# Kernel tuning notes

Hardware: AMD Instinct MI355X
Metric: run time of the kernel (lower is better)

## Reference

```python
import jax, jax.numpy as jnp
import numpy as np

NUM_GRAPHS = 5 * 0 + 64  # number of graphs in the batch
NUM_CLASSES = 5


def gcn_conv(x, src, dst, W, b, n_nodes):
    """PyG GCNConv: x' = D^{-1/2} (A+I) D^{-1/2} x W + b (self-loops already in src/dst)."""
    h = x @ W  # [N, out]
    deg = jax.ops.segment_sum(jnp.ones(dst.shape, h.dtype), dst, num_segments=n_nodes)
    dinv = deg ** -0.5  # deg >= 1 thanks to self-loops
    norm = dinv[src] * dinv[dst]  # [E+N]
    msg = h[src] * norm[:, None]  # gather + normalize
    out = jax.ops.segment_sum(msg, dst, num_segments=n_nodes)  # scatter-add
    return out + b


def setup_inputs() -> dict:
    key = jax.random.key(0)
    ks = jax.random.split(key, 12)
    N, E, D_IN, D_H, D_F = 50000, 500000, 128, 256, 256
    x = jax.random.normal(ks[0], (N, D_IN), dtype=jnp.float32)
    edge_index = jax.random.randint(ks[1], (2, E), 0, N, dtype=jnp.int64)
    batch = jnp.sort(jax.random.randint(ks[2], (N,), 0, NUM_GRAPHS, dtype=jnp.int64))
    def lin(k, fi, fo):
        s = 1.0 / np.sqrt(fi)
        return jax.random.uniform(k, (fi, fo), jnp.float32, -s, s)
    return {
        "x": x, "edge_index": edge_index, "batch": batch,
        "W0": lin(ks[3], D_IN, D_H), "b0": jnp.zeros((D_H,), jnp.float32),
        "W1": lin(ks[4], D_H, D_H),  "b1": jnp.zeros((D_H,), jnp.float32),
        "W2": lin(ks[5], D_H, D_H),  "b2": jnp.zeros((D_H,), jnp.float32),
        "Wc1": lin(ks[6], D_H, D_F), "bc1": jnp.zeros((D_F,), jnp.float32),
        "Wc2": lin(ks[7], D_F, NUM_CLASSES), "bc2": jnp.zeros((NUM_CLASSES,), jnp.float32),
    }


def reference(x, edge_index, batch, W0, b0, W1, b1, W2, b2, Wc1, bc1, Wc2, bc2):
    n_nodes = x.shape[0]
    loops = jnp.arange(n_nodes, dtype=edge_index.dtype)
    src = jnp.concatenate([edge_index[0], loops])
    dst = jnp.concatenate([edge_index[1], loops])

    h = jax.nn.relu(gcn_conv(x, src, dst, W0, b0, n_nodes))
    h = jax.nn.relu(gcn_conv(h, src, dst, W1, b1, n_nodes))
    h = jax.nn.relu(gcn_conv(h, src, dst, W2, b2, n_nodes))

    # global_mean_pool over batch ids
    sums = jax.ops.segment_sum(h, batch, num_segments=NUM_GRAPHS)
    cnts = jax.ops.segment_sum(jnp.ones((n_nodes,), h.dtype), batch, num_segments=NUM_GRAPHS)
    g = sums / jnp.maximum(cnts, 1.0)[:, None]  # [NUM_GRAPHS, D_H]

    # classifier MLP (dropout inactive at eval)
    out = jax.nn.relu(g @ Wc1 + bc1) @ Wc2 + bc2
    return out
```

## Files before the change

### kernel.cpp

```cpp
#include <hip/hip_runtime.h>
#include <hip/hip_fp16.h>

typedef _Float16 f16x8 __attribute__((ext_vector_type(8)));
typedef float fx4 __attribute__((ext_vector_type(4)));

#define AS_G(p) ((const __attribute__((address_space(1))) void*)(p))
#define AS_L(p) ((__attribute__((address_space(3))) void*)(p))

struct __align__(8) half4 { __half2 lo, hi; };
struct __align__(8) edge_t { int u; float w; };

__device__ inline void split2h(float a, __half& hi, __half& lo) {
    hi = __float2half(a);
    lo = __float2half(a - __half2float(hi));
}


__global__ void k_degx(const int* __restrict__ dst, int E, int* __restrict__ deg, int degB,
                       const float* __restrict__ x, __half* __restrict__ xh, int nx) {
    if (blockIdx.x < (unsigned)degB) {
        int i = (blockIdx.x * 256 + threadIdx.x) * 4;
        if (i + 4 <= E) {
            int4 d4 = *(const int4*)&dst[i];
            atomicAdd(&deg[d4.x], 1);
            atomicAdd(&deg[d4.y], 1);
            atomicAdd(&deg[d4.z], 1);
            atomicAdd(&deg[d4.w], 1);
        } else {
            for (int j = i; j < E; ++j) atomicAdd(&deg[dst[j]], 1);
        }
    } else {
        int i = (blockIdx.x - degB) * 1024 + threadIdx.x * 4;
        if (i < nx) {
            float4 v = *(const float4*)&x[i];
            __half2 h0(__float2half(v.x), __float2half(v.y));
            __half2 h1(__float2half(v.z), __float2half(v.w));
            *(__half2*)&xh[i] = h0;
            *(__half2*)&xh[i + 2] = h1;
        }
    }
}

__global__ void k_scan1w(const int* __restrict__ deg, int N, int nb,
                         int* __restrict__ part, int* __restrict__ bsum, float* __restrict__ dinv,
                         const float* __restrict__ W0, __half* __restrict__ h0, __half* __restrict__ l0,
                         const float* __restrict__ W1, __half* __restrict__ h1, __half* __restrict__ l1,
                         const float* __restrict__ W2, __half* __restrict__ h2, __half* __restrict__ l2,
                         int DIN, int DH) {
    __shared__ int s[256];
    if (blockIdx.x < (unsigned)nb) {
        int i = blockIdx.x * 256 + threadIdx.x;
        int v = (i < N) ? deg[i] : 0;
        if (i < N) dinv[i] = 1.0f / sqrtf((float)(v + 1));
        s[threadIdx.x] = v;
        __syncthreads();
        for (int off = 1; off < 256; off <<= 1) {
            int t = (threadIdx.x >= off) ? s[threadIdx.x - off] : 0;
            __syncthreads();
            s[threadIdx.x] += t;
            __syncthreads();
        }
        if (i < N) part[i] = s[threadIdx.x] - v;
        if (threadIdx.x == 255) bsum[blockIdx.x] = s[255];
    } else {
        int i = (blockIdx.x - nb) * 256 + threadIdx.x;
        const int n0 = DIN * DH, n1 = DH * DH;
        const float* W; __half *hT, *lT; int K, li;
        if (i < n0) { W = W0; hT = h0; lT = l0; K = DIN; li = i; }
        else if (i < n0 + n1) { W = W1; hT = h1; lT = l1; K = DH; li = i - n0; }
        else if (i < n0 + 2 * n1) { W = W2; hT = h2; lT = l2; K = DH; li = i - n0 - n1; }
        else return;
        int k = li / DH, n = li - k * DH;
        __half h, l;
        split2h(W[li], h, l);
        hT[(size_t)n * K + k] = h;
        lT[(size_t)n * K + k] = l;
    }
}

__global__ void k_scan3(const int* __restrict__ part, const int* __restrict__ bsum, int nb,
                        int N, int E, int* __restrict__ rowptr, int* __restrict__ cursor) {
    __shared__ int s[256];
    const int t = threadIdx.x;
    s[t] = (t < nb && t < (int)blockIdx.x) ? bsum[t] : 0;
    __syncthreads();
    for (int off = 128; off > 0; off >>= 1) {
        if (t < off) s[t] += s[t + off];
        __syncthreads();
    }
    const int base = s[0];
    int i = blockIdx.x * 256 + t;
    if (i < N) {
        int v = part[i] + base;
        rowptr[i] = v;
        cursor[i] = v;
    }
    if (i == 0) rowptr[N] = E;
}

__global__ void k_fill(const int* __restrict__ src, const int* __restrict__ dst, int E,
                       const float* __restrict__ dinv, int* __restrict__ cursor,
                       edge_t* __restrict__ edg) {
    int e = blockIdx.x * blockDim.x + threadIdx.x;
    if (e < E) {
        int s = src[e], d = dst[e];
        int p = atomicAdd(&cursor[d], 1);
        edge_t ed;
        ed.u = s;
        ed.w = dinv[s] * dinv[d];
        edg[p] = ed;
    }
}


__device__ __forceinline__ void gemm_core(
    const __half* __restrict__ Aop, const __half* __restrict__ BhiT, const __half* __restrict__ BloT,
    __half* smem, int Nrows, int K, int row0,
    int wid, int lane, int wrow, int wcol, int quad, int l16, fx4 (&acc)[4][4]) {
    const __half* gp[5];
    int ldsoff[5];
#pragma unroll
    for (int j = 0; j < 5; ++j) {
        int L = wid * 5 + j;
        int arr, slot;
        if (L < 8) { arr = 0; slot = L; }
        else if (L < 24) { arr = 1; slot = L - 8; }
        else { arr = 2; slot = L - 24; }
        int r = 16 * slot + (lane >> 2);
        int s = lane & 3;
        int q = (s - (r >> 1)) & 3;
        const __half* garr = (arr == 0) ? Aop : (arr == 1) ? BhiT : BloT;
        int grow = (arr == 0) ? min(row0 + r, Nrows - 1) : r;
        gp[j] = garr + (size_t)grow * K + q * 8;
        ldsoff[j] = ((arr == 0) ? 0 : (arr == 1) ? 8192 : 24576) + slot * 1024;
    }

    const __half* sA   = smem;
    const __half* sBhi = smem + 4096;
    const __half* sBlo = smem + 12288;

    int aidx[4], bidx[4];
#pragma unroll
    for (int t = 0; t < 4; ++t) {
        int ra = wrow * 64 + t * 16 + l16;
        aidx[t] = ra * 32 + ((quad + (ra >> 1)) & 3) * 8;
        int rb = wcol * 64 + t * 16 + l16;
        bidx[t] = rb * 32 + ((quad + (rb >> 1)) & 3) * 8;
    }

    for (int k0 = 0; k0 < K; k0 += 32) {
#pragma unroll
        for (int j = 0; j < 5; ++j)
            __builtin_amdgcn_global_load_lds(AS_G(gp[j] + k0), AS_L((char*)smem + ldsoff[j]), 16, 0, 0);
        __syncthreads();

        f16x8 a[4];
#pragma unroll
        for (int mi = 0; mi < 4; ++mi) a[mi] = *(const f16x8*)&sA[aidx[mi]];
#pragma unroll
        for (int nj = 0; nj < 4; ++nj) {
            f16x8 bh = *(const f16x8*)&sBhi[bidx[nj]];
            f16x8 bl = *(const f16x8*)&sBlo[bidx[nj]];
#pragma unroll
            for (int mi = 0; mi < 4; ++mi) {
                acc[mi][nj] = __builtin_amdgcn_mfma_f32_16x16x32_f16(a[mi], bh, acc[mi][nj], 0, 0, 0);
                acc[mi][nj] = __builtin_amdgcn_mfma_f32_16x16x32_f16(a[mi], bl, acc[mi][nj], 0, 0, 0);
            }
        }
        __syncthreads();
    }
}

__global__ __launch_bounds__(512) void k_gemm_mfma(
    const __half* __restrict__ Aop, const __half* __restrict__ BhiT, const __half* __restrict__ BloT,
    const float* __restrict__ bias, __half* __restrict__ C, int Nrows, int K) {
    __shared__ __align__(16) __half smem[20480];
    const int tid = threadIdx.x;
    const int wid = tid >> 6, lane = tid & 63;
    const int row0 = blockIdx.x * 128;
    const int wrow = wid & 1, wcol = wid >> 1;
    const int quad = lane >> 4, l16 = lane & 15;

    fx4 acc[4][4] = {};
    gemm_core(Aop, BhiT, BloT, smem, Nrows, K, row0, wid, lane, wrow, wcol, quad, l16, acc);

#pragma unroll
    for (int mi = 0; mi < 4; ++mi) {
        const int rbase = row0 + wrow * 64 + mi * 16 + quad * 4;
#pragma unroll
        for (int nj = 0; nj < 4; ++nj) {
            const int c = wcol * 64 + nj * 16 + l16;
            const float bc = bias[c];
#pragma unroll
            for (int reg = 0; reg < 4; ++reg) {
                int r = rbase + reg;
                if (r < Nrows) C[(size_t)r * 256 + c] = __float2half(fmaxf(acc[mi][nj][reg] + bc, 0.f));
            }
        }
    }
}

__global__ __launch_bounds__(512) void k_gemm_pool(
    const __half* __restrict__ Aop, const __half* __restrict__ BhiT, const __half* __restrict__ BloT,
    const float* __restrict__ bias, const int* __restrict__ batch,
    float* __restrict__ gsum, int Nrows, int K) {
    __shared__ __align__(16) __half smem[20480];
    const int tid = threadIdx.x;
    const int wid = tid >> 6, lane = tid & 63;
    const int row0 = blockIdx.x * 128;
    const int wrow = wid & 1, wcol = wid >> 1;
    const int quad = lane >> 4, l16 = lane & 15;

    fx4 acc[4][4] = {};
    gemm_core(Aop, BhiT, BloT, smem, Nrows, K, row0, wid, lane, wrow, wcol, quad, l16, acc);

    int bg[4][4];
#pragma unroll
    for (int mi = 0; mi < 4; ++mi)
#pragma unroll
        for (int reg = 0; reg < 4; ++reg) {
            int r = row0 + wrow * 64 + mi * 16 + quad * 4 + reg;
            bg[mi][reg] = (r < Nrows) ? batch[r] : -1;
        }
    const int gfirst = batch[row0 < Nrows ? row0 : (Nrows - 1)];
    const int glast  = batch[min(row0 + 127, Nrows - 1)];

#pragma unroll
    for (int nj = 0; nj < 4; ++nj) {
        const int c = wcol * 64 + nj * 16 + l16;
        const float bc = bias[c];
        for (int g = gfirst; g <= glast; ++g) {
            float s = 0.f;
#pragma unroll
            for (int mi = 0; mi < 4; ++mi)
#pragma unroll
                for (int reg = 0; reg < 4; ++reg)
                    if (bg[mi][reg] == g) s += fmaxf(acc[mi][nj][reg] + bc, 0.f);
            s += __shfl_xor(s, 16);
            s += __shfl_xor(s, 32);
            if (quad == 0) atomicAdd(&gsum[g * 256 + c], s);
        }
    }
}


__global__ __launch_bounds__(256) void k_agg256(const __half* __restrict__ H, const int* __restrict__ rowptr,
                                                const edge_t* __restrict__ edg,
                                                const float* __restrict__ dinv,
                                                __half* __restrict__ outA, int N) {
    const int wave = threadIdx.x >> 6, lane = threadIdx.x & 63;
    const int v = blockIdx.x * 4 + wave;
    if (v >= N) return;

    const float di = dinv[v];
    const float selfn = di * di;
    half4 hv = ((const half4*)&H[(size_t)v * 256])[lane];
    float2 s0 = __half22float2(hv.lo), s1 = __half22float2(hv.hi);
    float ax = selfn * s0.x, ay = selfn * s0.y, az = selfn * s1.x, aw = selfn * s1.y;

    int e = rowptr[v];
    const int end = rowptr[v + 1];
    for (; e + 8 <= end; e += 8) {
        edge_t ed[8]; half4 g[8];
#pragma unroll
        for (int j = 0; j < 8; ++j) ed[j] = edg[e + j];
#pragma unroll
        for (int j = 0; j < 8; ++j) g[j] = ((const half4*)&H[(size_t)ed[j].u * 256])[lane];
#pragma unroll
        for (int j = 0; j < 8; ++j) {
            float2 f0 = __half22float2(g[j].lo), f1 = __half22float2(g[j].hi);
            ax += ed[j].w * f0.x; ay += ed[j].w * f0.y; az += ed[j].w * f1.x; aw += ed[j].w * f1.y;
        }
    }
    for (; e < end; ++e) {
        edge_t ed = edg[e];
        half4 g = ((const half4*)&H[(size_t)ed.u * 256])[lane];
        float2 f0 = __half22float2(g.lo), f1 = __half22float2(g.hi);
        ax += ed.w * f0.x; ay += ed.w * f0.y; az += ed.w * f1.x; aw += ed.w * f1.y;
    }

    half4 o;
    o.lo = __floats2half2_rn(ax, ay);
    o.hi = __floats2half2_rn(az, aw);
    ((half4*)outA)[(size_t)v * 64 + lane] = o;
}

__global__ __launch_bounds__(256) void k_agg128(const __half* __restrict__ X, const int* __restrict__ rowptr,
                                                const edge_t* __restrict__ edg,
                                                const float* __restrict__ dinv,
                                                __half* __restrict__ outA, int N) {
    const int half = threadIdx.x >> 5, sub = threadIdx.x & 31;
    const int v = blockIdx.x * 8 + half;
    if (v >= N) return;

    const float di = dinv[v];
    const float selfn = di * di;
    half4 hv = ((const half4*)&X[(size_t)v * 128])[sub];
    float2 s0 = __half22float2(hv.lo), s1 = __half22float2(hv.hi);
    float ax = selfn * s0.x, ay = selfn * s0.y, az = selfn * s1.x, aw = selfn * s1.y;

    int e = rowptr[v];
    const int end = rowptr[v + 1];
    for (; e + 4 <= end; e += 4) {
        edge_t ed[4]; half4 g[4];
#pragma unroll
        for (int j = 0; j < 4; ++j) ed[j] = edg[e + j];
#pragma unroll
        for (int j = 0; j < 4; ++j) g[j] = ((const half4*)&X[(size_t)ed[j].u * 128])[sub];
#pragma unroll
        for (int j = 0; j < 4; ++j) {
            float2 f0 = __half22float2(g[j].lo), f1 = __half22float2(g[j].hi);
            ax += ed[j].w * f0.x; ay += ed[j].w * f0.y; az += ed[j].w * f1.x; aw += ed[j].w * f1.y;
        }
    }
    for (; e < end; ++e) {
        edge_t ed = edg[e];
        half4 g = ((const half4*)&X[(size_t)ed.u * 128])[sub];
        float2 f0 = __half22float2(g.lo), f1 = __half22float2(g.hi);
        ax += ed.w * f0.x; ay += ed.w * f0.y; az += ed.w * f1.x; aw += ed.w * f1.y;
    }

    half4 o;
    o.lo = __floats2half2_rn(ax, ay);
    o.hi = __floats2half2_rn(az, aw);
    ((half4*)outA)[(size_t)v * 32 + sub] = o;
}


__global__ __launch_bounds__(256) void k_poolcls(const float* __restrict__ gsum, const int* __restrict__ batch,
                                                 int N,
                                                 const float* __restrict__ Wc1, const float* __restrict__ bc1,
                                                 const float* __restrict__ Wc2, const float* __restrict__ bc2,
                                                 float* __restrict__ out) {
    __shared__ float sg[256], sh[256];
    __shared__ int bounds[2];
    const int b = blockIdx.x, t = threadIdx.x;
    if (t < 2) {
        int target = b + t;
        int lo = 0, hi = N;
        while (lo < hi) {
            int mid = (lo + hi) >> 1;
            if (batch[mid] < target) lo = mid + 1; else hi = mid;
        }
        bounds[t] = lo;
    }
    __syncthreads();
    const float c = (float)(bounds[1] - bounds[0]);
    sg[t] = gsum[b * 256 + t] / fmaxf(c, 1.0f);
    __syncthreads();
    float acc = bc1[t];
    for (int k = 0; k < 256; ++k) acc += sg[k] * Wc1[k * 256 + t];
    sh[t] = fmaxf(acc, 0.f);
    __syncthreads();
    if (t < 5) {
        float o = bc2[t];
        for (int k = 0; k < 256; ++k) o += sh[k] * Wc2[k * 5 + t];
        out[b * 5 + t] = o;
    }
}


extern "C" void kernel_launch(void* const* d_in, const int* in_sizes, int n_in,
                              void* d_out, int out_size, void* d_ws, size_t ws_size,
                              hipStream_t stream) {
    const float* x    = (const float*)d_in[0];
    const int*   eidx = (const int*)d_in[1];
    const int*   batch= (const int*)d_in[2];
    const float* W0 = (const float*)d_in[3];  const float* b0 = (const float*)d_in[4];
    const float* W1 = (const float*)d_in[5];  const float* b1 = (const float*)d_in[6];
    const float* W2 = (const float*)d_in[7];  const float* b2 = (const float*)d_in[8];
    const float* Wc1= (const float*)d_in[9];  const float* bc1= (const float*)d_in[10];
    const float* Wc2= (const float*)d_in[11]; const float* bc2= (const float*)d_in[12];
    float* out = (float*)d_out;

    const int N   = in_sizes[2];
    const int E   = in_sizes[1] / 2;
    const int DIN = in_sizes[0] / N;
    const int DH  = in_sizes[4];
    const int* src = eidx;
    const int* dst = eidx + E;

    char* p = (char*)d_ws;
    auto alloc = [&](size_t bytes) {
        char* r = p;
        p += (bytes + 255) & ~(size_t)255;
        return (void*)r;
    };
    __half* hbuf = (__half*)alloc((size_t)N * DH * 2);
    __half* ha   = (__half*)alloc((size_t)N * DH * 2);
    __half* xh   = (__half*)alloc((size_t)N * DIN * 2);
    __half* w0hi = (__half*)alloc((size_t)DH * DIN * 2);
    __half* w0lo = (__half*)alloc((size_t)DH * DIN * 2);
    __half* w1hi = (__half*)alloc((size_t)DH * DH * 2);
    __half* w1lo = (__half*)alloc((size_t)DH * DH * 2);
    __half* w2hi = (__half*)alloc((size_t)DH * DH * 2);
    __half* w2lo = (__half*)alloc((size_t)DH * DH * 2);
    int*   deg   = (int*)alloc((size_t)N * 4);
    float* gsum  = (float*)alloc(64 * (size_t)DH * 4);
    float* dinv  = (float*)alloc((size_t)N * 4);
    int*   part  = (int*)alloc((size_t)N * 4);
    int*   bsum  = (int*)alloc(256 * 4);
    int*   rowptr= (int*)alloc((size_t)(N + 1) * 4);
    int*   cursor= (int*)alloc((size_t)N * 4);
    edge_t* edg  = (edge_t*)alloc((size_t)E * 8);

    hipMemsetAsync(deg, 0, (size_t)((char*)gsum - (char*)deg) + 64 * (size_t)DH * 4, stream);

    const int nb = (N + 255) / 256;
    const int wtot = DIN * DH + 2 * DH * DH;
    const int wb = (wtot + 255) / 256;
    const int degB = (E + 1023) / 1024;
    const int nx = N * DIN;
    const int xb = (nx + 1023) / 1024;

    k_degx  <<<degB + xb, 256, 0, stream>>>(dst, E, deg, degB, x, xh, nx);
    k_scan1w<<<nb + wb, 256, 0, stream>>>(deg, N, nb, part, bsum, dinv,
                                          W0, w0hi, w0lo, W1, w1hi, w1lo, W2, w2hi, w2lo, DIN, DH);
    k_scan3 <<<nb, 256, 0, stream>>>(part, bsum, nb, N, E, rowptr, cursor);
    k_fill  <<<(E + 255) / 256, 256, 0, stream>>>(src, dst, E, dinv, cursor, edg);

    const int gemmBlocks = (N + 127) / 128;

    k_agg128<<<(N + 7) / 8, 256, 0, stream>>>(xh, rowptr, edg, dinv, ha, N);
    k_gemm_mfma<<<gemmBlocks, 512, 0, stream>>>(ha, w0hi, w0lo, b0, hbuf, N, DIN);
    k_agg256<<<(N + 3) / 4, 256, 0, stream>>>(hbuf, rowptr, edg, dinv, ha, N);
    k_gemm_mfma<<<gemmBlocks, 512, 0, stream>>>(ha, w1hi, w1lo, b1, hbuf, N, DH);
    k_agg256<<<(N + 3) / 4, 256, 0, stream>>>(hbuf, rowptr, edg, dinv, ha, N);
    k_gemm_pool<<<gemmBlocks, 512, 0, stream>>>(ha, w2hi, w2lo, b2, batch, gsum, N, DH);

    k_poolcls<<<64, 256, 0, stream>>>(gsum, batch, N, Wc1, bc1, Wc2, bc2, out);
}
```

Measured before the change: 340.2 us.

## Double-buffer A tile in LDS and load B fragments directly from global

The GEMM core now stages only the A tile in LDS, double-buffered so the next k-slice loads asynchronously while the current one is consumed, which leaves one barrier per iteration instead of two. The B hi/lo fragments are read straight from global memory into registers rather than through LDS, which shrinks shared memory from 40KB to 16KB per block and may raise occupancy. In exchange, every wave re-reads B from global/L2 with less coalesced 16-byte loads per lane. Correctness with a single barrier depends on the alternating buffers not being overwritten while another wave is still reading them.

```diff
diff --git a/kernel.cpp b/kernel.cpp
--- a/kernel.cpp
+++ b/kernel.cpp
@@ -117,64 +117,65 @@
     const __half* __restrict__ Aop, const __half* __restrict__ BhiT, const __half* __restrict__ BloT,
     __half* smem, int Nrows, int K, int row0,
     int wid, int lane, int wrow, int wcol, int quad, int l16, fx4 (&acc)[4][4]) {
-    const __half* gp[5];
-    int ldsoff[5];
-#pragma unroll
-    for (int j = 0; j < 5; ++j) {
-        int L = wid * 5 + j;
-        int arr, slot;
-        if (L < 8) { arr = 0; slot = L; }
-        else if (L < 24) { arr = 1; slot = L - 8; }
-        else { arr = 2; slot = L - 24; }
-        int r = 16 * slot + (lane >> 2);
-        int s = lane & 3;
-        int q = (s - (r >> 1)) & 3;
-        const __half* garr = (arr == 0) ? Aop : (arr == 1) ? BhiT : BloT;
-        int grow = (arr == 0) ? min(row0 + r, Nrows - 1) : r;
-        gp[j] = garr + (size_t)grow * K + q * 8;
-        ldsoff[j] = ((arr == 0) ? 0 : (arr == 1) ? 8192 : 24576) + slot * 1024;
-    }
-
-    const __half* sA   = smem;
-    const __half* sBhi = smem + 4096;
-    const __half* sBlo = smem + 12288;
-
-    int aidx[4], bidx[4];
+    const int r = 16 * wid + (lane >> 2);
+    const int s = lane & 3;
+    const int q = (s - (r >> 1)) & 3;
+    const __half* agp = Aop + (size_t)min(row0 + r, Nrows - 1) * K + q * 8;
+    const int aslot = wid * 1024;
+
+    const __half* bph[4];
+    const __half* bpl[4];
 #pragma unroll
     for (int t = 0; t < 4; ++t) {
-        int ra = wrow * 64 + t * 16 + l16;
+        const int rb = wcol * 64 + t * 16 + l16;
+        bph[t] = BhiT + (size_t)rb * K + quad * 8;
+        bpl[t] = BloT + (size_t)rb * K + quad * 8;
+    }
+
+    int aidx[4];
+#pragma unroll
+    for (int t = 0; t < 4; ++t) {
+        const int ra = wrow * 64 + t * 16 + l16;
         aidx[t] = ra * 32 + ((quad + (ra >> 1)) & 3) * 8;
-        int rb = wcol * 64 + t * 16 + l16;
-        bidx[t] = rb * 32 + ((quad + (rb >> 1)) & 3) * 8;
-    }
-
-    for (int k0 = 0; k0 < K; k0 += 32) {
-#pragma unroll
-        for (int j = 0; j < 5; ++j)
-            __builtin_amdgcn_global_load_lds(AS_G(gp[j] + k0), AS_L((char*)smem + ldsoff[j]), 16, 0, 0);
+    }
+
+    const int NI = K >> 5;
+    __builtin_amdgcn_global_load_lds(AS_G(agp), AS_L((char*)smem + aslot), 16, 0, 0);
+
+    for (int it = 0; it < NI; ++it) {
         __syncthreads();
-
+        const int k0 = it * 32;
+
+        f16x8 bh[4], bl[4];
+#pragma unroll
+        for (int nj = 0; nj < 4; ++nj) {
+            bh[nj] = *(const f16x8*)(bph[nj] + k0);
+            bl[nj] = *(const f16x8*)(bpl[nj] + k0);
+        }
+
+        if (it + 1 < NI)
+            __builtin_amdgcn_global_load_lds(AS_G(agp + (it + 1) * 32),
+                AS_L((char*)smem + (((it + 1) & 1) << 13) + aslot), 16, 0, 0);
+
+        const __half* sA = (const __half*)((const char*)smem + ((it & 1) << 13));
         f16x8 a[4];
 #pragma unroll
         for (int mi = 0; mi < 4; ++mi) a[mi] = *(const f16x8*)&sA[aidx[mi]];
-#pragma unroll
-        for (int nj = 0; nj < 4; ++nj) {
-            f16x8 bh = *(const f16x8*)&sBhi[bidx[nj]];
-            f16x8 bl = *(const f16x8*)&sBlo[bidx[nj]];
+
+#pragma unroll
+        for (int nj = 0; nj < 4; ++nj)
 #pragma unroll
             for (int mi = 0; mi < 4; ++mi) {
-                acc[mi][nj] = __builtin_amdgcn_mfma_f32_16x16x32_f16(a[mi], bh, acc[mi][nj], 0, 0, 0);
-                acc[mi][nj] = __builtin_amdgcn_mfma_f32_16x16x32_f16(a[mi], bl, acc[mi][nj], 0, 0, 0);
+                acc[mi][nj] = __builtin_amdgcn_mfma_f32_16x16x32_f16(a[mi], bh[nj], acc[mi][nj], 0, 0, 0);
+                acc[mi][nj] = __builtin_amdgcn_mfma_f32_16x16x32_f16(a[mi], bl[nj], acc[mi][nj], 0, 0, 0);
             }
-        }
-        __syncthreads();
     }
 }
 
 __global__ __launch_bounds__(512) void k_gemm_mfma(
     const __half* __restrict__ Aop, const __half* __restrict__ BhiT, const __half* __restrict__ BloT,
     const float* __restrict__ bias, __half* __restrict__ C, int Nrows, int K) {
-    __shared__ __align__(16) __half smem[20480];
+    __shared__ __align__(16) __half smem[8192];
     const int tid = threadIdx.x;
     const int wid = tid >> 6, lane = tid & 63;
     const int row0 = blockIdx.x * 128;
@@ -204,7 +205,7 @@
     const __half* __restrict__ Aop, const __half* __restrict__ BhiT, const __half* __restrict__ BloT,
     const float* __restrict__ bias, const int* __restrict__ batch,
     float* __restrict__ gsum, int Nrows, int K) {
-    __shared__ __align__(16) __half smem[20480];
+    __shared__ __align__(16) __half smem[8192];
     const int tid = threadIdx.x;
     const int wid = tid >> 6, lane = tid & 63;
     const int row0 = blockIdx.x * 128;
```

New measurement: 415.3 us. +22.1%, slower.
